# Optimization experiments

Measured on AMD Instinct MI355X. Metric: run time of the kernel, lower is better.

## Reference

```python
import jax, jax.numpy as jnp
import numpy as np

EMBED_DIM = 1024
B, S = 4, 2048
SCALE = float(np.sqrt(EMBED_DIM))


def setup_inputs() -> dict:
    key = jax.random.key(0)
    ks = jax.random.split(key, 9)
    d = EMBED_DIM
    init = 1.0 / np.sqrt(d)
    return {
        "query": jax.random.normal(ks[0], (B, S, d), jnp.float32),
        "key": jax.random.normal(ks[1], (B, S, d), jnp.float32),
        "value": jax.random.normal(ks[2], (B, S, d), jnp.float32),
        "wq": jax.random.uniform(ks[3], (d, d), jnp.float32, -init, init),
        "bq": jax.random.uniform(ks[4], (d,), jnp.float32, -init, init),
        "wk": jax.random.uniform(ks[5], (d, d), jnp.float32, -init, init),
        "bk": jax.random.uniform(ks[6], (d,), jnp.float32, -init, init),
        "wv": jax.random.uniform(ks[7], (d, d), jnp.float32, -init, init),
        "bv": jax.random.uniform(ks[8], (d,), jnp.float32, -init, init),
    }


def reference(query, key, value, wq, bq, wk, bk, wv, bv):
    # Linear projections (torch Linear: x @ W^T + b; here weights stored as [in, out])
    q = query @ wq + bq            # [B,S,D]
    k = key @ wk + bk              # [B,S,D]
    v = value @ wv + bv            # [B,S,D]
    scores = jnp.einsum("bqd,bkd->bqk", q, k) / SCALE   # [B,S,S]
    attn = jax.nn.softmax(scores, axis=-1)
    # dropout in eval mode -> identity
    return jnp.einsum("bqk,bkd->bqd", attn, v)          # [B,S,D]
```

## Files before the change

kernel.cpp:

```cpp
#include <hip/hip_runtime.h>
#include <hip/hip_bf16.h>

typedef __attribute__((ext_vector_type(4))) float   f32x4;
typedef __attribute__((ext_vector_type(8))) __bf16  bf16x8;
typedef __attribute__((ext_vector_type(4))) __bf16  bf16x4;

#define NB 4
#define SS 2048
#define DD 1024

__device__ __forceinline__ void gload_lds16(const void* g, void* l) {
  __builtin_amdgcn_global_load_lds((const __attribute__((address_space(1))) void*)g,
                                   (__attribute__((address_space(3))) void*)l,
                                   16, 0, 0);
}

__global__ __launch_bounds__(256) void prep_w_kernel(
    const float* __restrict__ wq, const float* __restrict__ wk, const float* __restrict__ wv,
    const float* __restrict__ bq, const float* __restrict__ bk, const float* __restrict__ bv,
    __bf16* __restrict__ Wt, float* __restrict__ biasbuf)
{
  const int z = blockIdx.z;
  const float* W  = z == 0 ? wq : (z == 1 ? wk : wv);
  const float* bi = z == 0 ? bq : (z == 1 ? bk : bv);
  __bf16* dst = Wt + (size_t)z * (size_t)(DD * DD);
  const int n0 = blockIdx.x * 32, k0 = blockIdx.y * 32;
  __shared__ float t[32][33];
  const int tx = threadIdx.x & 31, ty = threadIdx.x >> 5;
  #pragma unroll
  for (int i = 0; i < 4; i++)
    t[ty + 8 * i][tx] = W[(size_t)(k0 + ty + 8 * i) * DD + n0 + tx];
  __syncthreads();
  #pragma unroll
  for (int i = 0; i < 4; i++)
    dst[(size_t)(n0 + ty + 8 * i) * DD + k0 + tx] = (__bf16)t[tx][ty + 8 * i];
  if (blockIdx.x == 0 && blockIdx.y == 0) {
    #pragma unroll
    for (int i = 0; i < 4; i++)
      biasbuf[z * DD + threadIdx.x + 256 * i] = bi[threadIdx.x + 256 * i];
  }
}

#define A2_OFF(BUF)      ((BUF) * 16384)
#define B2_OFF(BUF, NH)  (32768 + ((BUF)*2 + (NH)) * 16384)

#define DSREAD_A2(BUF)                                                          \
  _Pragma("unroll") for (int mi = 0; mi < 4; ++mi) {                            \
    _Pragma("unroll") for (int ks = 0; ks < 2; ++ks)                            \
      af[mi][ks] = *(const bf16x8*)(smem + A2_OFF(BUF) + ara[ks] + mi * 2048); }

#define DSREAD_B2(DST, BUF, NH)                                                 \
  _Pragma("unroll") for (int ni = 0; ni < 2; ++ni) {                            \
    _Pragma("unroll") for (int ks = 0; ks < 2; ++ks)                            \
      DST[ni][ks] = *(const bf16x8*)(smem + B2_OFF(BUF, NH) + brb2[ks] + ni * 2048); }


#define PJ_GLA(V0, V1, V2, V3, T) do { int t_ = (T); if (t_ >= 16) t_ = 0;      \
  const float* g_ = Ablk + (size_t)t_ * 64;                                     \
  V0 = *(const float4*)(g_ + aoffF0); V1 = *(const float4*)(g_ + aoffF0 + 4);   \
  V2 = *(const float4*)(g_ + aoffF1); V3 = *(const float4*)(g_ + aoffF1 + 4);   \
  __builtin_amdgcn_sched_barrier(0); } while (0)

#define PJ_WRA(BUF, V0, V1, V2, V3) do {                                        \
  bf16x8 w0_, w1_;                                                              \
  w0_[0]=(__bf16)V0.x; w0_[1]=(__bf16)V0.y; w0_[2]=(__bf16)V0.z; w0_[3]=(__bf16)V0.w; \
  w0_[4]=(__bf16)V1.x; w0_[5]=(__bf16)V1.y; w0_[6]=(__bf16)V1.z; w0_[7]=(__bf16)V1.w; \
  w1_[0]=(__bf16)V2.x; w1_[1]=(__bf16)V2.y; w1_[2]=(__bf16)V2.z; w1_[3]=(__bf16)V2.w; \
  w1_[4]=(__bf16)V3.x; w1_[5]=(__bf16)V3.y; w1_[6]=(__bf16)V3.z; w1_[7]=(__bf16)V3.w; \
  *(bf16x8*)(smem + A2_OFF(BUF) + tid * 16) = w0_;                              \
  *(bf16x8*)(smem + A2_OFF(BUF) + 8192 + tid * 16) = w1_; } while (0)

#define PJ_SB0(BUF, T) do { int t_ = (T); if (t_ >= 16) t_ = 0;                 \
  const __bf16* gB_ = Bblk + (size_t)t_ * 64;                                   \
  gload_lds16(gB_ + boff0, smem + B2_OFF(BUF, 0) + tid * 16);                   \
  gload_lds16(gB_ + boff1, smem + B2_OFF(BUF, 0) + 8192 + tid * 16); } while (0)

#define PJ_SB1(BUF, T) do { int t_ = (T); if (t_ >= 16) t_ = 0;                 \
  const __bf16* gB_ = Bblk + (size_t)(128 * 1024) + (size_t)t_ * 64;            \
  gload_lds16(gB_ + boff0, smem + B2_OFF(BUF, 1) + tid * 16);                   \
  gload_lds16(gB_ + boff1, smem + B2_OFF(BUF, 1) + 8192 + tid * 16); } while (0)

#define PJ_MFMA(BF, NH) do {                                                    \
  __builtin_amdgcn_s_barrier();                                                 \
  asm volatile("s_waitcnt lgkmcnt(0)" ::: "memory");                            \
  __builtin_amdgcn_sched_barrier(0);                                            \
  __builtin_amdgcn_s_setprio(1);                                                \
  _Pragma("unroll") for (int mi = 0; mi < 4; ++mi)                              \
  _Pragma("unroll") for (int ni = 0; ni < 2; ++ni)                              \
  _Pragma("unroll") for (int ks = 0; ks < 2; ++ks)                              \
    acc[mi][(NH)*2+ni] = __builtin_amdgcn_mfma_f32_16x16x32_bf16(               \
        af[mi][ks], BF[ni][ks], acc[mi][(NH)*2+ni], 0, 0, 0);                   \
  __builtin_amdgcn_s_setprio(0);                                                \
  __builtin_amdgcn_sched_barrier(0);                                            \
  __builtin_amdgcn_s_barrier(); } while (0)

__global__ __launch_bounds__(512) void proj_kernel(
    const float* __restrict__ Xq, const float* __restrict__ Xk, const float* __restrict__ Xv,
    const __bf16* __restrict__ Wt, const float* __restrict__ bias,
    __bf16* __restrict__ Qo, __bf16* __restrict__ Ko, __bf16* __restrict__ Vt)
{
  extern __shared__ char smem[];

  const int gx = gridDim.x, gy = gridDim.y;
  const int nwg = gx * gy * gridDim.z;
  int lin = blockIdx.x + gx * (blockIdx.y + gy * blockIdx.z);
  const int cpx = nwg >> 3;
  int swz = (lin & 7) * cpx + (lin >> 3);
  const int bx = swz % gx;
  int rem = swz / gx;
  const int by = rem % gy;
  const int bz = rem / gy;

  const long brow = (long)by * 128, bcol = (long)bx * 256;
  const float* Xsel = bz == 0 ? Xq : (bz == 1 ? Xk : Xv);
  const float* Ablk = Xsel + (size_t)brow * 1024;
  const __bf16* Bblk = Wt + (size_t)bz * (DD * DD) + (size_t)bcol * 1024;

  const int tid  = threadIdx.x;
  const int lane = tid & 63;
  const int wid  = tid >> 6;
  const int wm = wid >> 2, wn = wid & 3;
  const int l15 = lane & 15, l4 = lane >> 4;
  const int lx = (lane & 7) << 4;

  const int niter = 8;

  int aoffF0, aoffF1, boff0, boff1;
  #pragma unroll
  for (int i = 0; i < 2; ++i) {
    const int p = i * 8192 + tid * 16;
    const int r = p >> 7;
    const int kb = (p ^ ((r & 7) << 4)) & 127;
    const int aF = r * 1024 + (kb >> 1);
    const int bO = r * 1024 + (kb >> 1);
    if (i == 0) { aoffF0 = aF; boff0 = bO; } else { aoffF1 = aF; boff1 = bO; }
  }

  int ara[2], brb2[2];
  #pragma unroll
  for (int ks = 0; ks < 2; ++ks) {
    ara[ks]  = ((((wm * 64 + l15) * 64 + l4 * 8) * 2) + ks * 64) ^ lx;
    brb2[ks] = ((((wn * 32 + l15) * 64 + l4 * 8) * 2) + ks * 64) ^ lx;
  }

  f32x4 acc[4][4] = {};
  bf16x8 af[4][2], b0[2][2], b1[2][2];
  float4 La0, La1, La2, La3, Lb0, Lb1, Lb2, Lb3;

  PJ_GLA(La0, La1, La2, La3, 0);
  PJ_SB0(0, 0); PJ_SB1(0, 0); PJ_SB0(1, 1);
  PJ_GLA(Lb0, Lb1, Lb2, Lb3, 1);
  asm volatile("s_waitcnt vmcnt(10)" ::: "memory");
  PJ_WRA(0, La0, La1, La2, La3);
  asm volatile("s_waitcnt vmcnt(0)" ::: "memory");
  PJ_WRA(1, Lb0, Lb1, Lb2, Lb3);
  asm volatile("s_waitcnt lgkmcnt(0)" ::: "memory");
  __builtin_amdgcn_s_barrier();

  for (int it = 0; it < niter; ++it) {
    const int tt = it * 2;
    PJ_GLA(La0, La1, La2, La3, tt + 2);
    PJ_SB1(1, tt + 1);
    DSREAD_A2(0); DSREAD_B2(b0, 0, 0);
    PJ_MFMA(b0, 0);
    asm volatile("s_waitcnt vmcnt(2)" ::: "memory");
    PJ_WRA(0, La0, La1, La2, La3);
    PJ_SB0(0, tt + 2);
    DSREAD_B2(b1, 0, 1);
    PJ_MFMA(b1, 1);
    PJ_GLA(Lb0, Lb1, Lb2, Lb3, tt + 3);
    PJ_SB1(0, tt + 2);
    DSREAD_A2(1); DSREAD_B2(b0, 1, 0);
    PJ_MFMA(b0, 0);
    asm volatile("s_waitcnt vmcnt(2)" ::: "memory");
    PJ_WRA(1, Lb0, Lb1, Lb2, Lb3);
    PJ_SB0(1, tt + 3);
    DSREAD_B2(b1, 1, 1);
    PJ_MFMA(b1, 1);
  }

  if (bz == 2) {
    #pragma unroll
    for (int mi = 0; mi < 4; ++mi) {
      #pragma unroll
      for (int n = 0; n < 4; ++n) {
        const long row = brow + wm * 64 + mi * 16 + l4 * 4;
        const long col = bcol + (n >> 1) * 128 + wn * 32 + (n & 1) * 16 + l15;
        const float bvv = bias[2 * DD + col];
        const long bb = row >> 11, s = row & 2047;
        bf16x4 pk = { (__bf16)(acc[mi][n][0] + bvv), (__bf16)(acc[mi][n][1] + bvv),
                      (__bf16)(acc[mi][n][2] + bvv), (__bf16)(acc[mi][n][3] + bvv) };
        *(bf16x4*)&Vt[bb * 2097152 + col * 2048 + s] = pk;
      }
    }
  } else {
    __bf16* C = bz == 0 ? Qo : Ko;
    #pragma unroll
    for (int mi = 0; mi < 4; ++mi) {
      #pragma unroll
      for (int n = 0; n < 4; ++n) {
        const long row = brow + wm * 64 + mi * 16 + l4 * 4;
        const long col = bcol + (n >> 1) * 128 + wn * 32 + (n & 1) * 16 + l15;
        const float bvv = bias[bz * DD + col];
        #pragma unroll
        for (int e = 0; e < 4; ++e)
          C[(row + e) * 1024 + col] = (__bf16)(acc[mi][n][e] + bvv);
      }
    }
  }
}


#define A_OFF(BUF, MH) (((BUF)*2 + (MH)) * 16384)
#define B_OFF(BUF, NH) (65536 + ((BUF)*2 + (NH)) * 16384)

#define STAGE_A(BUF, MH, T) do { int t_ = (T); if (t_ >= NT) t_ = 0;            \
  const __bf16* gs_ = Ablk + (size_t)(MH) * (64 * (size_t)lda) + (size_t)t_ * 64; \
  gload_lds16(gs_ + aoff0, smem + A_OFF(BUF, MH) + tid * 16);                    \
  gload_lds16(gs_ + aoff1, smem + A_OFF(BUF, MH) + 8192 + tid * 16); } while (0)

#define STAGE_B(BUF, NH, T) do { int t_ = (T); if (t_ >= NT) t_ = 0;            \
  const __bf16* gs_ = Bblk + (size_t)(NH) * (32 * (size_t)ldb) + (size_t)t_ * 64; \
  gload_lds16(gs_ + boff0, smem + B_OFF(BUF, NH) + tid * 16);                    \
  gload_lds16(gs_ + boff1, smem + B_OFF(BUF, NH) + 8192 + tid * 16); } while (0)

#define DSREAD_A(DST, BUF, MH)                                                  \
  _Pragma("unroll") for (int mi = 0; mi < 4; ++mi) {                            \
    _Pragma("unroll") for (int ks = 0; ks < 2; ++ks)                            \
      DST[mi][ks] = *(const bf16x8*)(smem + A_OFF(BUF, MH) + arb[ks] + mi * 2048); }

#define DSREAD_B(DST, BUF, NH)                                                  \
  _Pragma("unroll") for (int ni = 0; ni < 2; ++ni) {                            \
    _Pragma("unroll") for (int ks = 0; ks < 2; ++ks)                            \
      DST[ni][ks] = *(const bf16x8*)(smem + B_OFF(BUF, NH) + brb[ks] + ni * 2048); }

#define BARRIER_MFMA(AF, BF, MH, NH) do {                                       \
  __builtin_amdgcn_s_barrier();                                                 \
  asm volatile("s_waitcnt lgkmcnt(0)" ::: "memory");                            \
  __builtin_amdgcn_sched_barrier(0);                                            \
  __builtin_amdgcn_s_setprio(1);                                                \
  _Pragma("unroll") for (int mi = 0; mi < 4; ++mi)                              \
  _Pragma("unroll") for (int ni = 0; ni < 2; ++ni)                              \
  _Pragma("unroll") for (int ks = 0; ks < 2; ++ks)                              \
    acc[(MH)*4+mi][(NH)*2+ni] = __builtin_amdgcn_mfma_f32_16x16x32_bf16(        \
        AF[mi][ks], BF[ni][ks], acc[(MH)*4+mi][(NH)*2+ni], 0, 0, 0);            \
  __builtin_amdgcn_s_setprio(0);                                                \
  __builtin_amdgcn_sched_barrier(0);                                            \
  __builtin_amdgcn_s_barrier(); } while (0)

__global__ __launch_bounds__(512) void gemm8p_kernel(
    const __bf16* __restrict__ A, const __bf16* __restrict__ B,
    float scale, void* __restrict__ Cout,
    int K, int lda, int ldb, int ldc,
    long strideA, long strideB, long strideC)
{
  extern __shared__ char smem[];

  const int gx = gridDim.x, gy = gridDim.y;
  const int nwg = gx * gy * gridDim.z;
  int lin = blockIdx.x + gx * (blockIdx.y + gy * blockIdx.z);
  const int cpx = nwg >> 3;
  int swz = (lin & 7) * cpx + (lin >> 3);
  const int bx = swz % gx;
  int rem = swz / gx;
  const int by = rem % gy;
  const int bz = rem / gy;

  const long brow = (long)by * 256, bcol = (long)bx * 256;
  const __bf16* Ablk = A + (size_t)bz * strideA + (size_t)brow * lda;
  const __bf16* Bblk = B + (size_t)bz * strideB + (size_t)bcol * ldb;

  const int tid  = threadIdx.x;
  const int lane = tid & 63;
  const int wid  = tid >> 6;
  const int wm = wid >> 2, wn = wid & 3;
  const int l15 = lane & 15, l4 = lane >> 4;
  const int lx = (lane & 7) << 4;

  const int NT = K >> 6;
  const int niter = NT >> 1;

  int aoff0, aoff1, boff0, boff1;
  #pragma unroll
  for (int i = 0; i < 2; ++i) {
    const int p = i * 8192 + tid * 16;
    const int l = p ^ (((p >> 7) & 7) << 4);
    const int r = p >> 7;
    const int kb = l & 127;
    const int av = ((r >> 6) * 128 + (r & 63)) * lda + (kb >> 1);
    const int bv = ((r >> 5) * 64 + (r & 31)) * ldb + (kb >> 1);
    if (i == 0) { aoff0 = av; boff0 = bv; } else { aoff1 = av; boff1 = bv; }
  }

  int arb[2], brb[2];
  #pragma unroll
  for (int ks = 0; ks < 2; ++ks) {
    arb[ks] = ((((wm * 64 + l15) * 64 + l4 * 8) * 2) + ks * 64) ^ lx;
    brb[ks] = ((((wn * 32 + l15) * 64 + l4 * 8) * 2) + ks * 64) ^ lx;
  }

  f32x4 acc[8][4] = {};
  bf16x8 a0[4][2], a1[4][2], b0[2][2], b1[2][2];

  STAGE_B(0, 0, 0); STAGE_A(0, 0, 0); STAGE_A(0, 1, 0); STAGE_B(0, 1, 0);
  STAGE_B(1, 0, 1); STAGE_A(1, 0, 1);
  asm volatile("s_waitcnt vmcnt(4)" ::: "memory");
  __builtin_amdgcn_s_barrier();

  for (int it = 0; it < niter; ++it) {
    const int tt = it * 2;
    DSREAD_A(a0, 0, 0); DSREAD_B(b0, 0, 0);
    STAGE_A(1, 1, tt + 1);
    BARRIER_MFMA(a0, b0, 0, 0);
    DSREAD_A(a1, 0, 1);
    STAGE_B(1, 1, tt + 1);
    BARRIER_MFMA(a1, b0, 1, 0);
    DSREAD_B(b1, 0, 1);
    STAGE_B(0, 0, tt + 2);
    BARRIER_MFMA(a0, b1, 0, 1);
    STAGE_A(0, 0, tt + 2);
    asm volatile("s_waitcnt vmcnt(4)" ::: "memory");
    BARRIER_MFMA(a1, b1, 1, 1);
    DSREAD_A(a0, 1, 0); DSREAD_B(b0, 1, 0);
    STAGE_A(0, 1, tt + 2);
    BARRIER_MFMA(a0, b0, 0, 0);
    DSREAD_A(a1, 1, 1);
    STAGE_B(0, 1, tt + 2);
    BARRIER_MFMA(a1, b0, 1, 0);
    DSREAD_B(b1, 1, 1);
    STAGE_B(1, 0, tt + 3);
    BARRIER_MFMA(a0, b1, 0, 1);
    STAGE_A(1, 0, tt + 3);
    asm volatile("s_waitcnt vmcnt(4)" ::: "memory");
    BARRIER_MFMA(a1, b1, 1, 1);
  }

  const int cr = l4 * 4;
  __bf16* C = (__bf16*)Cout + (size_t)bz * strideC;
  #pragma unroll
  for (int m = 0; m < 8; ++m) {
    #pragma unroll
    for (int n = 0; n < 4; ++n) {
      const long row = brow + wm * 128 + m * 16 + cr;
      const long col = bcol + wn * 64 + n * 16 + l15;
      #pragma unroll
      for (int e = 0; e < 4; ++e)
        C[(row + e) * (size_t)ldc + col] = (__bf16)__expf(acc[m][n][e] * scale);
    }
  }
}


#define STAGE_SA(BUF, T) do { int t_ = (T); if (t_ >= NT) t_ = 0;              \
  const __bf16* gA_ = Ablk + (size_t)t_ * 64;                                   \
  gload_lds16(gA_ + aoff0, smem + A2_OFF(BUF) + tid * 16);                      \
  gload_lds16(gA_ + aoff1, smem + A2_OFF(BUF) + 8192 + tid * 16);               \
  const __bf16* gB_ = Bblk + (size_t)t_ * 64;                                   \
  gload_lds16(gB_ + boff0, smem + B2_OFF(BUF, 0) + tid * 16);                   \
  gload_lds16(gB_ + boff1, smem + B2_OFF(BUF, 0) + 8192 + tid * 16); } while (0)

#define STAGE_SB(BUF, T) do { int t_ = (T); if (t_ >= NT) t_ = 0;              \
  const __bf16* gB_ = Bblk + (size_t)(128 * (size_t)ldb) + (size_t)t_ * 64;     \
  gload_lds16(gB_ + boff0, smem + B2_OFF(BUF, 1) + tid * 16);                   \
  gload_lds16(gB_ + boff1, smem + B2_OFF(BUF, 1) + 8192 + tid * 16); } while (0)

#define MFMA2(BF, NH, DOSUM) do {                                               \
  __builtin_amdgcn_s_barrier();                                                 \
  asm volatile("s_waitcnt lgkmcnt(0)" ::: "memory");                            \
  __builtin_amdgcn_sched_barrier(0);                                            \
  __builtin_amdgcn_s_setprio(1);                                                \
  _Pragma("unroll") for (int mi = 0; mi < 4; ++mi)                              \
  _Pragma("unroll") for (int ni = 0; ni < 2; ++ni)                              \
  _Pragma("unroll") for (int ks = 0; ks < 2; ++ks)                              \
    acc[mi][(NH)*2+ni] = __builtin_amdgcn_mfma_f32_16x16x32_bf16(               \
        af[mi][ks], BF[ni][ks], acc[mi][(NH)*2+ni], 0, 0, 0);                   \
  if (DOSUM) {                                                                  \
    _Pragma("unroll") for (int mi = 0; mi < 4; ++mi)                            \
    _Pragma("unroll") for (int ks = 0; ks < 2; ++ks)                            \
      accs[mi] = __builtin_amdgcn_mfma_f32_16x16x32_bf16(                       \
          af[mi][ks], onesf, accs[mi], 0, 0, 0); }                              \
  __builtin_amdgcn_s_setprio(0);                                                \
  __builtin_amdgcn_sched_barrier(0);                                            \
  __builtin_amdgcn_s_barrier(); } while (0)

__global__ __launch_bounds__(512) void gemm128_kernel(
    const __bf16* __restrict__ A, const __bf16* __restrict__ B,
    void* __restrict__ Cout,
    int K, int lda, int ldb, int ldc,
    long strideA, long strideB, long strideC)
{
  extern __shared__ char smem[];

  const int gx = gridDim.x, gy = gridDim.y;
  const int nwg = gx * gy * gridDim.z;
  int lin = blockIdx.x + gx * (blockIdx.y + gy * blockIdx.z);
  const int cpx = nwg >> 3;
  int swz = (lin & 7) * cpx + (lin >> 3);
  const int bx = swz % gx;
  int rem = swz / gx;
  const int by = rem % gy;
  const int bz = rem / gy;

  const long brow = (long)by * 128, bcol = (long)bx * 256;
  const __bf16* Ablk = A + (size_t)bz * strideA + (size_t)brow * lda;
  const __bf16* Bblk = B + (size_t)bz * strideB + (size_t)bcol * ldb;

  const int tid  = threadIdx.x;
  const int lane = tid & 63;
  const int wid  = tid >> 6;
  const int wm = wid >> 2, wn = wid & 3;
  const int l15 = lane & 15, l4 = lane >> 4;
  const int lx = (lane & 7) << 4;

  const int NT = K >> 6;
  const int niter = NT >> 1;

  int aoff0, aoff1, boff0, boff1;
  #pragma unroll
  for (int i = 0; i < 2; ++i) {
    const int p = i * 8192 + tid * 16;
    const int r = p >> 7;
    const int kb = (p ^ ((r & 7) << 4)) & 127;
    const int av = r * lda + (kb >> 1);
    const int bv = r * ldb + (kb >> 1);
    if (i == 0) { aoff0 = av; boff0 = bv; } else { aoff1 = av; boff1 = bv; }
  }

  int ara[2], brb2[2];
  #pragma unroll
  for (int ks = 0; ks < 2; ++ks) {
    ara[ks]  = ((((wm * 64 + l15) * 64 + l4 * 8) * 2) + ks * 64) ^ lx;
    brb2[ks] = ((((wn * 32 + l15) * 64 + l4 * 8) * 2) + ks * 64) ^ lx;
  }

  f32x4 acc[4][4] = {};
  f32x4 accs[4] = {};
  bf16x8 af[4][2], b0[2][2], b1[2][2];
  bf16x8 onesf;
  #pragma unroll
  for (int j = 0; j < 8; ++j) onesf[j] = (__bf16)1.0f;

  STAGE_SA(0, 0); STAGE_SB(0, 0); STAGE_SA(1, 1);
  asm volatile("s_waitcnt vmcnt(6)" ::: "memory");
  __builtin_amdgcn_s_barrier();

  for (int it = 0; it < niter; ++it) {
    const int tt = it * 2;
    STAGE_SB(1, tt + 1);
    asm volatile("s_waitcnt vmcnt(6)" ::: "memory");
    DSREAD_A2(0); DSREAD_B2(b0, 0, 0);
    MFMA2(b0, 0, 1);
    STAGE_SA(0, tt + 2);
    asm volatile("s_waitcnt vmcnt(6)" ::: "memory");
    DSREAD_B2(b1, 0, 1);
    MFMA2(b1, 1, 0);
    STAGE_SB(0, tt + 2);
    asm volatile("s_waitcnt vmcnt(6)" ::: "memory");
    DSREAD_A2(1); DSREAD_B2(b0, 1, 0);
    MFMA2(b0, 0, 1);
    STAGE_SA(1, tt + 3);
    asm volatile("s_waitcnt vmcnt(6)" ::: "memory");
    DSREAD_B2(b1, 1, 1);
    MFMA2(b1, 1, 0);
  }

  float* C = (float*)Cout + (size_t)bz * strideC;
  #pragma unroll
  for (int mi = 0; mi < 4; ++mi) {
    f32x4 inv;
    #pragma unroll
    for (int e = 0; e < 4; ++e) inv[e] = 1.0f / accs[mi][e];
    #pragma unroll
    for (int n = 0; n < 4; ++n) {
      const long row = brow + wm * 64 + mi * 16 + l4 * 4;
      const long col = bcol + (n >> 1) * 128 + wn * 32 + (n & 1) * 16 + l15;
      #pragma unroll
      for (int e = 0; e < 4; ++e)
        C[(row + e) * (size_t)ldc + col] = acc[mi][n][e] * inv[e];
    }
  }
}

extern "C" void kernel_launch(void* const* d_in, const int* in_sizes, int n_in,
                              void* d_out, int out_size, void* d_ws, size_t ws_size,
                              hipStream_t stream)
{
  const float* query = (const float*)d_in[0];
  const float* key   = (const float*)d_in[1];
  const float* value = (const float*)d_in[2];
  const float* wq = (const float*)d_in[3];
  const float* bq = (const float*)d_in[4];
  const float* wk = (const float*)d_in[5];
  const float* bk = (const float*)d_in[6];
  const float* wv = (const float*)d_in[7];
  const float* bv = (const float*)d_in[8];

  char* ws = (char*)d_ws;
  __bf16* P       = (__bf16*)(ws + 0);
  __bf16* Wt      = (__bf16*)(ws + 33554432);
  float*  biasbuf = (float*)(ws + 39845888);
  __bf16* Qb      = (__bf16*)(ws + 39858176);
  __bf16* Kb      = (__bf16*)(ws + 56635392);
  __bf16* Vt      = (__bf16*)(ws + 73412608);

  hipFuncSetAttribute((const void*)proj_kernel,    hipFuncAttributeMaxDynamicSharedMemorySize, 131072);
  hipFuncSetAttribute((const void*)gemm8p_kernel,  hipFuncAttributeMaxDynamicSharedMemorySize, 131072);
  hipFuncSetAttribute((const void*)gemm128_kernel, hipFuncAttributeMaxDynamicSharedMemorySize, 131072);

  dim3 b256(256), b512(512);

  prep_w_kernel<<<dim3(32, 32, 3), b256, 0, stream>>>(wq, wk, wv, bq, bk, bv, Wt, biasbuf);

  proj_kernel<<<dim3(4, 64, 3), b512, 98304, stream>>>(
      query, key, value, Wt, biasbuf, Qb, Kb, Vt);

  gemm8p_kernel<<<dim3(8, 8, 4), b512, 131072, stream>>>(
      Qb, Kb, 0.03125f, P,
      1024, 1024, 1024, 2048,
      2097152L, 2097152L, 4194304L);

  gemm128_kernel<<<dim3(4, 16, 4), b512, 98304, stream>>>(
      P, Vt, d_out,
      2048, 2048, 2048, 1024,
      4194304L, 2097152L, 2097152L);

  (void)in_sizes; (void)n_in; (void)out_size; (void)ws_size;
}
```

Before: 172.2 us.

## Stage fp32 projection inputs directly into LDS and convert to bf16 on read

The projection kernel used to load fp32 activations into registers, convert them to bf16, and write them to LDS. It now uses async global-to-LDS loads to stage the raw fp32 A tiles in a swizzled layout, and converts to bf16 while reading LDS for the MFMA operands. The aim is to remove register staging and the explicit LDS stores, so A loads travel the same async path as B and overlap with compute. In exchange the A tile uses twice the LDS (dynamic shared memory goes from 96KB to 128KB), which may reduce occupancy and doubles LDS read traffic for A; the PV kernel macros are renamed to avoid clashes.

```diff
diff --git a/kernel.cpp b/kernel.cpp
--- a/kernel.cpp
+++ b/kernel.cpp
@@ -41,41 +41,36 @@
   }
 }
 
-#define A2_OFF(BUF)      ((BUF) * 16384)
-#define B2_OFF(BUF, NH)  (32768 + ((BUF)*2 + (NH)) * 16384)
-
-#define DSREAD_A2(BUF)                                                          \
-  _Pragma("unroll") for (int mi = 0; mi < 4; ++mi) {                            \
-    _Pragma("unroll") for (int ks = 0; ks < 2; ++ks)                            \
-      af[mi][ks] = *(const bf16x8*)(smem + A2_OFF(BUF) + ara[ks] + mi * 2048); }
+
+#define A32_OFF(BUF)     ((BUF) * 32768)
+#define B2_OFF(BUF, NH)  (65536 + ((BUF)*2 + (NH)) * 16384)
 
 #define DSREAD_B2(DST, BUF, NH)                                                 \
   _Pragma("unroll") for (int ni = 0; ni < 2; ++ni) {                            \
     _Pragma("unroll") for (int ks = 0; ks < 2; ++ks)                            \
       DST[ni][ks] = *(const bf16x8*)(smem + B2_OFF(BUF, NH) + brb2[ks] + ni * 2048); }
 
-
-#define PJ_GLA(V0, V1, V2, V3, T) do { int t_ = (T); if (t_ >= 16) t_ = 0;      \
-  const float* g_ = Ablk + (size_t)t_ * 64;                                     \
-  V0 = *(const float4*)(g_ + aoffF0); V1 = *(const float4*)(g_ + aoffF0 + 4);   \
-  V2 = *(const float4*)(g_ + aoffF1); V3 = *(const float4*)(g_ + aoffF1 + 4);   \
-  __builtin_amdgcn_sched_barrier(0); } while (0)
-
-#define PJ_WRA(BUF, V0, V1, V2, V3) do {                                        \
-  bf16x8 w0_, w1_;                                                              \
-  w0_[0]=(__bf16)V0.x; w0_[1]=(__bf16)V0.y; w0_[2]=(__bf16)V0.z; w0_[3]=(__bf16)V0.w; \
-  w0_[4]=(__bf16)V1.x; w0_[5]=(__bf16)V1.y; w0_[6]=(__bf16)V1.z; w0_[7]=(__bf16)V1.w; \
-  w1_[0]=(__bf16)V2.x; w1_[1]=(__bf16)V2.y; w1_[2]=(__bf16)V2.z; w1_[3]=(__bf16)V2.w; \
-  w1_[4]=(__bf16)V3.x; w1_[5]=(__bf16)V3.y; w1_[6]=(__bf16)V3.z; w1_[7]=(__bf16)V3.w; \
-  *(bf16x8*)(smem + A2_OFF(BUF) + tid * 16) = w0_;                              \
-  *(bf16x8*)(smem + A2_OFF(BUF) + 8192 + tid * 16) = w1_; } while (0)
-
-#define PJ_SB0(BUF, T) do { int t_ = (T); if (t_ >= 16) t_ = 0;                 \
+#define DSREAD_A32(BUF)                                                         \
+  _Pragma("unroll") for (int mi = 0; mi < 4; ++mi) {                            \
+    _Pragma("unroll") for (int ks = 0; ks < 2; ++ks) {                          \
+      f32x4 u_ = *(const f32x4*)(smem + A32_OFF(BUF) + a32lo[ks] + mi * 4096);  \
+      f32x4 v_ = *(const f32x4*)(smem + A32_OFF(BUF) + a32hi[ks] + mi * 4096);  \
+      bf16x8 r_;                                                                \
+      r_[0]=(__bf16)u_[0]; r_[1]=(__bf16)u_[1]; r_[2]=(__bf16)u_[2]; r_[3]=(__bf16)u_[3]; \
+      r_[4]=(__bf16)v_[0]; r_[5]=(__bf16)v_[1]; r_[6]=(__bf16)v_[2]; r_[7]=(__bf16)v_[3]; \
+      af[mi][ks] = r_; } }
+
+#define PJ_SA(BUF, T) do { int t_ = (T); if (t_ >= 16) t_ = 0;                  \
+  const float* gA_ = Ablk + (size_t)t_ * 64;                                    \
+  gload_lds16(gA_ + aof0, smem + A32_OFF(BUF) + tid * 16);                      \
+  gload_lds16(gA_ + aof1, smem + A32_OFF(BUF) + 8192 + tid * 16);               \
+  gload_lds16(gA_ + aof2, smem + A32_OFF(BUF) + 16384 + tid * 16);              \
+  gload_lds16(gA_ + aof3, smem + A32_OFF(BUF) + 24576 + tid * 16);              \
   const __bf16* gB_ = Bblk + (size_t)t_ * 64;                                   \
   gload_lds16(gB_ + boff0, smem + B2_OFF(BUF, 0) + tid * 16);                   \
   gload_lds16(gB_ + boff1, smem + B2_OFF(BUF, 0) + 8192 + tid * 16); } while (0)
 
-#define PJ_SB1(BUF, T) do { int t_ = (T); if (t_ >= 16) t_ = 0;                 \
+#define PJ_SB(BUF, T) do { int t_ = (T); if (t_ >= 16) t_ = 0;                  \
   const __bf16* gB_ = Bblk + (size_t)(128 * 1024) + (size_t)t_ * 64;            \
   gload_lds16(gB_ + boff0, smem + B2_OFF(BUF, 1) + tid * 16);                   \
   gload_lds16(gB_ + boff1, smem + B2_OFF(BUF, 1) + 8192 + tid * 16); } while (0)
@@ -123,58 +118,61 @@
   const int l15 = lane & 15, l4 = lane >> 4;
   const int lx = (lane & 7) << 4;
 
-  const int niter = 8;
-
-  int aoffF0, aoffF1, boff0, boff1;
+  int aof0, aof1, aof2, aof3;
+  #pragma unroll
+  for (int i = 0; i < 4; ++i) {
+    const int p = i * 8192 + tid * 16;
+    const int r = p >> 8;
+    const int kb = (p ^ ((r & 7) << 4)) & 255;
+    const int off = r * 1024 + (kb >> 2);
+    if (i == 0) aof0 = off; else if (i == 1) aof1 = off;
+    else if (i == 2) aof2 = off; else aof3 = off;
+  }
+  int boff0, boff1;
   #pragma unroll
   for (int i = 0; i < 2; ++i) {
     const int p = i * 8192 + tid * 16;
     const int r = p >> 7;
     const int kb = (p ^ ((r & 7) << 4)) & 127;
-    const int aF = r * 1024 + (kb >> 1);
-    const int bO = r * 1024 + (kb >> 1);
-    if (i == 0) { aoffF0 = aF; boff0 = bO; } else { aoffF1 = aF; boff1 = bO; }
-  }
-
-  int ara[2], brb2[2];
+    const int off = r * 1024 + (kb >> 1);
+    if (i == 0) boff0 = off; else boff1 = off;
+  }
+
+  int a32lo[2], a32hi[2];
   #pragma unroll
   for (int ks = 0; ks < 2; ++ks) {
-    ara[ks]  = ((((wm * 64 + l15) * 64 + l4 * 8) * 2) + ks * 64) ^ lx;
+    const int rowb = (wm * 64 + l15) * 256;
+    a32lo[ks] = rowb + ((l4 * 32 + ks * 128) ^ lx);
+    a32hi[ks] = rowb + ((l4 * 32 + ks * 128 + 16) ^ lx);
+  }
+  int brb2[2];
+  #pragma unroll
+  for (int ks = 0; ks < 2; ++ks)
     brb2[ks] = ((((wn * 32 + l15) * 64 + l4 * 8) * 2) + ks * 64) ^ lx;
-  }
 
   f32x4 acc[4][4] = {};
   bf16x8 af[4][2], b0[2][2], b1[2][2];
-  float4 La0, La1, La2, La3, Lb0, Lb1, Lb2, Lb3;
-
-  PJ_GLA(La0, La1, La2, La3, 0);
-  PJ_SB0(0, 0); PJ_SB1(0, 0); PJ_SB0(1, 1);
-  PJ_GLA(Lb0, Lb1, Lb2, Lb3, 1);
-  asm volatile("s_waitcnt vmcnt(10)" ::: "memory");
-  PJ_WRA(0, La0, La1, La2, La3);
-  asm volatile("s_waitcnt vmcnt(0)" ::: "memory");
-  PJ_WRA(1, Lb0, Lb1, Lb2, Lb3);
-  asm volatile("s_waitcnt lgkmcnt(0)" ::: "memory");
+
+  PJ_SA(0, 0); PJ_SB(0, 0); PJ_SA(1, 1);
+  asm volatile("s_waitcnt vmcnt(6)" ::: "memory");
   __builtin_amdgcn_s_barrier();
 
-  for (int it = 0; it < niter; ++it) {
+  for (int it = 0; it < 8; ++it) {
     const int tt = it * 2;
-    PJ_GLA(La0, La1, La2, La3, tt + 2);
-    PJ_SB1(1, tt + 1);
-    DSREAD_A2(0); DSREAD_B2(b0, 0, 0);
+    PJ_SB(1, tt + 1);
+    asm volatile("s_waitcnt vmcnt(10)" ::: "memory");
+    DSREAD_A32(0); DSREAD_B2(b0, 0, 0);
     PJ_MFMA(b0, 0);
-    asm volatile("s_waitcnt vmcnt(2)" ::: "memory");
-    PJ_WRA(0, La0, La1, La2, La3);
-    PJ_SB0(0, tt + 2);
+    PJ_SA(0, tt + 2);
+    asm volatile("s_waitcnt vmcnt(14)" ::: "memory");
     DSREAD_B2(b1, 0, 1);
     PJ_MFMA(b1, 1);
-    PJ_GLA(Lb0, Lb1, Lb2, Lb3, tt + 3);
-    PJ_SB1(0, tt + 2);
-    DSREAD_A2(1); DSREAD_B2(b0, 1, 0);
+    PJ_SB(0, tt + 2);
+    asm volatile("s_waitcnt vmcnt(10)" ::: "memory");
+    DSREAD_A32(1); DSREAD_B2(b0, 1, 0);
     PJ_MFMA(b0, 0);
-    asm volatile("s_waitcnt vmcnt(2)" ::: "memory");
-    PJ_WRA(1, Lb0, Lb1, Lb2, Lb3);
-    PJ_SB0(1, tt + 3);
+    PJ_SA(1, tt + 3);
+    asm volatile("s_waitcnt vmcnt(14)" ::: "memory");
     DSREAD_B2(b1, 1, 1);
     PJ_MFMA(b1, 1);
   }
@@ -229,7 +227,7 @@
     _Pragma("unroll") for (int ks = 0; ks < 2; ++ks)                            \
       DST[mi][ks] = *(const bf16x8*)(smem + A_OFF(BUF, MH) + arb[ks] + mi * 2048); }
 
-#define DSREAD_B(DST, BUF, NH)                                                  \
+#define DSREAD_BS(DST, BUF, NH)                                                 \
   _Pragma("unroll") for (int ni = 0; ni < 2; ++ni) {                            \
     _Pragma("unroll") for (int ks = 0; ks < 2; ++ks)                            \
       DST[ni][ks] = *(const bf16x8*)(smem + B_OFF(BUF, NH) + brb[ks] + ni * 2048); }
@@ -309,25 +307,25 @@
 
   for (int it = 0; it < niter; ++it) {
     const int tt = it * 2;
-    DSREAD_A(a0, 0, 0); DSREAD_B(b0, 0, 0);
+    DSREAD_A(a0, 0, 0); DSREAD_BS(b0, 0, 0);
     STAGE_A(1, 1, tt + 1);
     BARRIER_MFMA(a0, b0, 0, 0);
     DSREAD_A(a1, 0, 1);
     STAGE_B(1, 1, tt + 1);
     BARRIER_MFMA(a1, b0, 1, 0);
-    DSREAD_B(b1, 0, 1);
+    DSREAD_BS(b1, 0, 1);
     STAGE_B(0, 0, tt + 2);
     BARRIER_MFMA(a0, b1, 0, 1);
     STAGE_A(0, 0, tt + 2);
     asm volatile("s_waitcnt vmcnt(4)" ::: "memory");
     BARRIER_MFMA(a1, b1, 1, 1);
-    DSREAD_A(a0, 1, 0); DSREAD_B(b0, 1, 0);
+    DSREAD_A(a0, 1, 0); DSREAD_BS(b0, 1, 0);
     STAGE_A(0, 1, tt + 2);
     BARRIER_MFMA(a0, b0, 0, 0);
     DSREAD_A(a1, 1, 1);
     STAGE_B(0, 1, tt + 2);
     BARRIER_MFMA(a1, b0, 1, 0);
-    DSREAD_B(b1, 1, 1);
+    DSREAD_BS(b1, 1, 1);
     STAGE_B(1, 0, tt + 3);
     BARRIER_MFMA(a0, b1, 0, 1);
     STAGE_A(1, 0, tt + 3);
@@ -351,20 +349,33 @@
 }
 
 
-#define STAGE_SA(BUF, T) do { int t_ = (T); if (t_ >= NT) t_ = 0;              \
+#define PV_A_OFF(BUF)     ((BUF) * 16384)
+#define PV_B_OFF(BUF, NH) (32768 + ((BUF)*2 + (NH)) * 16384)
+
+#define PV_DSA(BUF)                                                             \
+  _Pragma("unroll") for (int mi = 0; mi < 4; ++mi) {                            \
+    _Pragma("unroll") for (int ks = 0; ks < 2; ++ks)                            \
+      af[mi][ks] = *(const bf16x8*)(smem + PV_A_OFF(BUF) + ara[ks] + mi * 2048); }
+
+#define PV_DSB(DST, BUF, NH)                                                    \
+  _Pragma("unroll") for (int ni = 0; ni < 2; ++ni) {                            \
+    _Pragma("unroll") for (int ks = 0; ks < 2; ++ks)                            \
+      DST[ni][ks] = *(const bf16x8*)(smem + PV_B_OFF(BUF, NH) + brb2[ks] + ni * 2048); }
+
+#define PV_SA(BUF, T) do { int t_ = (T); if (t_ >= NT) t_ = 0;                  \
   const __bf16* gA_ = Ablk + (size_t)t_ * 64;                                   \
-  gload_lds16(gA_ + aoff0, smem + A2_OFF(BUF) + tid * 16);                      \
-  gload_lds16(gA_ + aoff1, smem + A2_OFF(BUF) + 8192 + tid * 16);               \
+  gload_lds16(gA_ + aoff0, smem + PV_A_OFF(BUF) + tid * 16);                    \
+  gload_lds16(gA_ + aoff1, smem + PV_A_OFF(BUF) + 8192 + tid * 16);             \
   const __bf16* gB_ = Bblk + (size_t)t_ * 64;                                   \
-  gload_lds16(gB_ + boff0, smem + B2_OFF(BUF, 0) + tid * 16);                   \
-  gload_lds16(gB_ + boff1, smem + B2_OFF(BUF, 0) + 8192 + tid * 16); } while (0)
-
-#define STAGE_SB(BUF, T) do { int t_ = (T); if (t_ >= NT) t_ = 0;              \
+  gload_lds16(gB_ + boff0, smem + PV_B_OFF(BUF, 0) + tid * 16);                 \
+  gload_lds16(gB_ + boff1, smem + PV_B_OFF(BUF, 0) + 8192 + tid * 16); } while (0)
+
+#define PV_SB(BUF, T) do { int t_ = (T); if (t_ >= NT) t_ = 0;                  \
   const __bf16* gB_ = Bblk + (size_t)(128 * (size_t)ldb) + (size_t)t_ * 64;     \
-  gload_lds16(gB_ + boff0, smem + B2_OFF(BUF, 1) + tid * 16);                   \
-  gload_lds16(gB_ + boff1, smem + B2_OFF(BUF, 1) + 8192 + tid * 16); } while (0)
-
-#define MFMA2(BF, NH, DOSUM) do {                                               \
+  gload_lds16(gB_ + boff0, smem + PV_B_OFF(BUF, 1) + tid * 16);                 \
+  gload_lds16(gB_ + boff1, smem + PV_B_OFF(BUF, 1) + 8192 + tid * 16); } while (0)
+
+#define PV_MFMA(BF, NH, DOSUM) do {                                             \
   __builtin_amdgcn_s_barrier();                                                 \
   asm volatile("s_waitcnt lgkmcnt(0)" ::: "memory");                            \
   __builtin_amdgcn_sched_barrier(0);                                            \
@@ -440,28 +451,28 @@
   #pragma unroll
   for (int j = 0; j < 8; ++j) onesf[j] = (__bf16)1.0f;
 
-  STAGE_SA(0, 0); STAGE_SB(0, 0); STAGE_SA(1, 1);
+  PV_SA(0, 0); PV_SB(0, 0); PV_SA(1, 1);
   asm volatile("s_waitcnt vmcnt(6)" ::: "memory");
   __builtin_amdgcn_s_barrier();
 
   for (int it = 0; it < niter; ++it) {
     const int tt = it * 2;
-    STAGE_SB(1, tt + 1);
+    PV_SB(1, tt + 1);
     asm volatile("s_waitcnt vmcnt(6)" ::: "memory");
-    DSREAD_A2(0); DSREAD_B2(b0, 0, 0);
-    MFMA2(b0, 0, 1);
-    STAGE_SA(0, tt + 2);
+    PV_DSA(0); PV_DSB(b0, 0, 0);
+    PV_MFMA(b0, 0, 1);
+    PV_SA(0, tt + 2);
     asm volatile("s_waitcnt vmcnt(6)" ::: "memory");
-    DSREAD_B2(b1, 0, 1);
-    MFMA2(b1, 1, 0);
-    STAGE_SB(0, tt + 2);
+    PV_DSB(b1, 0, 1);
+    PV_MFMA(b1, 1, 0);
+    PV_SB(0, tt + 2);
     asm volatile("s_waitcnt vmcnt(6)" ::: "memory");
-    DSREAD_A2(1); DSREAD_B2(b0, 1, 0);
-    MFMA2(b0, 0, 1);
-    STAGE_SA(1, tt + 3);
+    PV_DSA(1); PV_DSB(b0, 1, 0);
+    PV_MFMA(b0, 0, 1);
+    PV_SA(1, tt + 3);
     asm volatile("s_waitcnt vmcnt(6)" ::: "memory");
-    DSREAD_B2(b1, 1, 1);
-    MFMA2(b1, 1, 0);
+    PV_DSB(b1, 1, 1);
+    PV_MFMA(b1, 1, 0);
   }
 
   float* C = (float*)Cout + (size_t)bz * strideC;
@@ -511,7 +522,7 @@
 
   prep_w_kernel<<<dim3(32, 32, 3), b256, 0, stream>>>(wq, wk, wv, bq, bk, bv, Wt, biasbuf);
 
-  proj_kernel<<<dim3(4, 64, 3), b512, 98304, stream>>>(
+  proj_kernel<<<dim3(4, 64, 3), b512, 131072, stream>>>(
       query, key, value, Wt, biasbuf, Qb, Kb, Vt);
 
   gemm8p_kernel<<<dim3(8, 8, 4), b512, 131072, stream>>>(
```

Measured after the change: 173.6 us. No clear change (+0.8%).
